# Performance work log

Measured on AMD Instinct MI355X. Metric: run time of the kernel, lower is better.

The kernel has to match this reference:

```python
import jax, jax.numpy as jnp
import numpy as np

TOP_K = 2

def setup_inputs() -> dict:
    key = jax.random.key(0)
    ks = jax.random.split(key, 8)
    B, T, C, E, I, S = 1, 2048, 2048, 8, 1408, 2816
    s = 0.02  # weight scale for numerical stability
    return {
        "x": jax.random.normal(ks[0], (B, T, C), jnp.float32),
        "gate_w": jax.random.normal(ks[1], (E, C), jnp.float32) * s,
        "w1": jax.random.normal(ks[2], (E, I, C), jnp.float32) * s,
        "w3": jax.random.normal(ks[3], (E, I, C), jnp.float32) * s,
        "w2": jax.random.normal(ks[4], (E, C, I), jnp.float32) * s,
        "sw1": jax.random.normal(ks[5], (S, C), jnp.float32) * s,
        "sw3": jax.random.normal(ks[6], (S, C), jnp.float32) * s,
        "sw2": jax.random.normal(ks[7], (C, S), jnp.float32) * s,
    }

def reference(x, gate_w, w1, w3, w2, sw1, sw3, sw2):
    B, T, C = x.shape
    E = gate_w.shape[0]
    xf = x.reshape(-1, C)                      # [N, C]
    N = xf.shape[0]
    # --- routing: top-k of raw logits, softmax over the k selected logits ---
    logits = xf @ gate_w.T                     # [N, E]
    pv, idx = jax.lax.top_k(logits, TOP_K)     # [N, K]
    pv = jax.nn.softmax(pv.astype(jnp.float32), axis=-1).astype(x.dtype)
    # token-expert combine weights (sum of probs per expert, scatter of top-k)
    tew = jnp.zeros((N, E), x.dtype).at[jnp.arange(N)[:, None], idx].add(pv)
    # --- experts (SwiGLU), computed densely over all experts and masked by tew ---
    h = jax.nn.silu(jnp.einsum('nc,eic->nei', xf, w1)) * jnp.einsum('nc,eic->nei', xf, w3)
    eo = jnp.einsum('nei,eci->nec', h, w2)     # [N, E, C]
    y = jnp.einsum('nec,ne->nc', eo, tew).reshape(B, T, C)
    # --- shared expert on the residual input ---
    sh = (jax.nn.silu(x @ sw1.T) * (x @ sw3.T)) @ sw2.T
    return y + sh
```

## Files before the change

### kernel.cpp

```cpp
#include <hip/hip_runtime.h>

#define DEVI __device__ __forceinline__

typedef __attribute__((ext_vector_type(4))) float f32x4;
typedef __attribute__((ext_vector_type(8))) short bf16x8;

static constexpr int NT = 2048;
static constexpr int CD = 2048;
static constexpr int NE = 8;
static constexpr int ID = 1408;
static constexpr int SD = 2816;
static constexpr int ROWS = 2 * NT;
static constexpr int ROWS_PAD = ROWS + 256;

DEVI unsigned short f2bf(float f) {
  unsigned u = __builtin_bit_cast(unsigned, f);
  u += 0x7fff + ((u >> 16) & 1);
  return (unsigned short)(u >> 16);
}
DEVI float bf2f(unsigned short s) { return __builtin_bit_cast(float, (unsigned)s << 16); }
DEVI float silu_f(float z) { return z / (1.f + __expf(-z)); }

DEVI void gll16(const void* g, void* l) {
  __builtin_amdgcn_global_load_lds((__attribute__((address_space(1))) void*)(void*)g,
                                   (__attribute__((address_space(3))) void*)l, 16, 0, 0);
}

DEVI void bar_sched() {
  __builtin_amdgcn_s_barrier();
  __builtin_amdgcn_sched_barrier(0);
}
DEVI void sched0() { __builtin_amdgcn_sched_barrier(0); }
DEVI void wait_vm8() { asm volatile("s_waitcnt vmcnt(8)" ::: "memory"); }
DEVI void wait_vm0() { asm volatile("s_waitcnt vmcnt(0)" ::: "memory"); }
DEVI void wait_lgk0() { asm volatile("s_waitcnt lgkmcnt(0)" ::: "memory"); }

DEVI int swz8(int bid, int nwg) {
  constexpr int CH = 8, G = 64;
  int nfull = nwg - (nwg % G);
  if (bid >= nfull) return bid;
  int c = bid / G, r = bid % G;
  return c * G + (r % 8) * CH + (r / 8);
}
DEVI int swz_chunk(int bid, int nwg) {
  constexpr int CH = 16, G = 8 * CH;
  int nfull = nwg - (nwg % G);
  if (bid >= nfull) return bid;
  int c = bid / G, r = bid % G;
  return c * G + (r % 8) * CH + (r / 8);
}

__global__ __launch_bounds__(256) void k_cvt(const float* __restrict__ s,
                                             unsigned short* __restrict__ d, int n8)
{
  int i = blockIdx.x * 256 + threadIdx.x;
  int stride = gridDim.x * 256;
  for (; i < n8; i += stride) {
    float4 a = ((const float4*)s)[2 * i];
    float4 b = ((const float4*)s)[2 * i + 1];
    ushort4 p0 = make_ushort4(f2bf(a.x), f2bf(a.y), f2bf(a.z), f2bf(a.w));
    ushort4 p1 = make_ushort4(f2bf(b.x), f2bf(b.y), f2bf(b.z), f2bf(b.w));
    ((ushort4*)d)[2 * i]     = p0;
    ((ushort4*)d)[2 * i + 1] = p1;
  }
}

__global__ __launch_bounds__(64) void k_router(const float* __restrict__ x,
    const float* __restrict__ gw, int* __restrict__ counts,
    int* __restrict__ eidx, int* __restrict__ posn, float* __restrict__ probs)
{
  const int n = blockIdx.x;
  const int lane = threadIdx.x;
  const float4* xr = (const float4*)(x + (size_t)n * CD);
  float acc[NE];
#pragma unroll
  for (int e = 0; e < NE; ++e) acc[e] = 0.f;
  for (int i = lane; i < CD / 4; i += 64) {
    float4 xv = xr[i];
#pragma unroll
    for (int e = 0; e < NE; ++e) {
      float4 gv = ((const float4*)(gw + (size_t)e * CD))[i];
      acc[e] += xv.x * gv.x + xv.y * gv.y + xv.z * gv.z + xv.w * gv.w;
    }
  }
#pragma unroll
  for (int e = 0; e < NE; ++e) {
    float v = acc[e];
#pragma unroll
    for (int off = 32; off > 0; off >>= 1) v += __shfl_down(v, off);
    acc[e] = v;
  }
  if (lane == 0) {
    int b0 = 0; float m0 = acc[0];
#pragma unroll
    for (int e = 1; e < NE; ++e) if (acc[e] > m0) { m0 = acc[e]; b0 = e; }
    int b1 = -1; float m1 = 0.f;
#pragma unroll
    for (int e = 0; e < NE; ++e) {
      if (e == b0) continue;
      if (b1 < 0 || acc[e] > m1) { m1 = acc[e]; b1 = e; }
    }
    float d = __expf(m1 - m0);
    float inv = 1.f / (1.f + d);
    eidx[2 * n] = b0; eidx[2 * n + 1] = b1;
    probs[2 * n] = inv; probs[2 * n + 1] = d * inv;
    posn[2 * n] = atomicAdd(&counts[b0], 1);
    posn[2 * n + 1] = atomicAdd(&counts[b1], 1);
  }
}

__global__ void k_scan(const int* __restrict__ counts, int* __restrict__ bases) {
  if (threadIdx.x == 0) {
    int s = 0;
    for (int e = 0; e < NE; ++e) { bases[e] = s; s += counts[e]; }
  }
}

__global__ __launch_bounds__(256) void k_build(const int* __restrict__ eidx,
    const int* __restrict__ posn, const int* __restrict__ bases,
    int* __restrict__ rows_of, int* __restrict__ row2tok)
{
  int n = blockIdx.x * 256 + threadIdx.x;
  if (n >= NT) return;
#pragma unroll
  for (int k = 0; k < 2; ++k) {
    int e = eidx[2 * n + k];
    int row = bases[e] + posn[2 * n + k];
    rows_of[2 * n + k] = row;
    row2tok[row] = n;
  }
}

__global__ __launch_bounds__(512, 2) void k_up(
    const unsigned short* __restrict__ xb,
    const unsigned short* __restrict__ w1b, const unsigned short* __restrict__ w3b,
    const unsigned short* __restrict__ sw1b, const unsigned short* __restrict__ sw3b,
    unsigned short* __restrict__ h, unsigned short* __restrict__ hs,
    const int* __restrict__ counts, const int* __restrict__ bases,
    const int* __restrict__ row2tok)
{
  extern __shared__ char sm[];
  constexpr int NSH = (NT / 256) * (SD / 128);
  constexpr int NWG = NSH + NE * (ID / 128) * (NT / 256);
  constexpr int NSTEP = CD / 64;

  int lin = swz8((int)blockIdx.x, NWG);
  int cls, mx, pn, e = 0;
  if (lin < NSH) { cls = 0; mx = lin % 8; pn = lin / 8; }
  else { cls = 1; int r = lin - NSH; mx = r % 8; r /= 8; pn = r % 11; e = r / 11; }

  int M = NT, baserow = 0;
  if (cls) { M = counts[e]; if (mx * 256 >= M) return; baserow = bases[e]; }
  const int m0 = mx * 256, n0 = pn * 128;

  const unsigned short* B1 = cls ? w1b + ((size_t)e * ID + n0) * CD : sw1b + (size_t)n0 * CD;
  const unsigned short* B3 = cls ? w3b + ((size_t)e * ID + n0) * CD : sw3b + (size_t)n0 * CD;

  const int tid = threadIdx.x, l = tid & 63, w = tid >> 6;
  const int wr = w >> 2, wn = w & 3;
  const int slot = ((tid & 7) ^ ((tid >> 3) & 7)) * 16;

  const char* aP[4];
#pragma unroll
  for (int t = 0; t < 4; ++t) {
    int r = t * 64 + (tid >> 3);
    const unsigned short* rb;
    if (cls) {
      int grow = m0 + r; int gr = grow < M ? grow : 0;
      rb = xb + (size_t)row2tok[baserow + gr] * CD;
    } else {
      rb = xb + (size_t)(m0 + r) * CD;
    }
    aP[t] = (const char*)rb + slot;
  }
  const char* bP1[2]; const char* bP3[2];
#pragma unroll
  for (int t = 0; t < 2; ++t) {
    int r = t * 64 + (tid >> 3);
    bP1[t] = (const char*)(B1 + (size_t)r * CD) + slot;
    bP3[t] = (const char*)(B3 + (size_t)r * CD) + slot;
  }

  f32x4 acc1[8][2], acc3[8][2];
#pragma unroll
  for (int m = 0; m < 8; ++m)
#pragma unroll
    for (int n = 0; n < 2; ++n) {
      acc1[m][n] = {0.f, 0.f, 0.f, 0.f};
      acc3[m][n] = {0.f, 0.f, 0.f, 0.f};
    }

  const int lrow = l & 15, lkg = l >> 4, l7 = l & 7;

  auto stage_first = [&](char* base, size_t kb) {
#pragma unroll
    for (int t = 0; t < 4; ++t) gll16(aP[t] + kb, base + t * 8192 + tid * 16);
  };
  auto stage_second = [&](char* base, size_t kb) {
    char* sB1 = base + 32768; char* sB3 = base + 49152;
#pragma unroll
    for (int t = 0; t < 2; ++t) {
      gll16(bP1[t] + kb, sB1 + t * 8192 + tid * 16);
      gll16(bP3[t] + kb, sB3 + t * 8192 + tid * 16);
    }
  };
  auto ldq = [&](bf16x8* fa, bf16x8* fb1, bf16x8* fb3, const char* cur, int mh, int kk) {
    const char* sA = cur; const char* sB1 = cur + 32768; const char* sB3 = cur + 49152;
    const int ao = ((kk * 4 + lkg) ^ l7) * 16;
#pragma unroll
    for (int m = 0; m < 4; ++m)
      fa[m] = *(const bf16x8*)(sA + (wr * 128 + mh * 64 + m * 16 + lrow) * 128 + ao);
#pragma unroll
    for (int n = 0; n < 2; ++n) {
      fb1[n] = *(const bf16x8*)(sB1 + (wn * 32 + n * 16 + lrow) * 128 + ao);
      fb3[n] = *(const bf16x8*)(sB3 + (wn * 32 + n * 16 + lrow) * 128 + ao);
    }
  };
  auto mmq = [&](const bf16x8* fa, const bf16x8* fb1, const bf16x8* fb3, int mh) {
    __builtin_amdgcn_s_setprio(1);
#pragma unroll
    for (int n = 0; n < 2; ++n)
#pragma unroll
      for (int m = 0; m < 4; ++m) {
        acc1[mh * 4 + m][n] = __builtin_amdgcn_mfma_f32_16x16x32_bf16(fa[m], fb1[n], acc1[mh * 4 + m][n], 0, 0, 0);
        acc3[mh * 4 + m][n] = __builtin_amdgcn_mfma_f32_16x16x32_bf16(fa[m], fb3[n], acc3[mh * 4 + m][n], 0, 0, 0);
      }
    __builtin_amdgcn_s_setprio(0);
  };

  stage_first(sm, 0);
  stage_second(sm, 0);
  wait_vm0(); bar_sched();

  bf16x8 Xa[4], Xb1[2], Xb3[2], Ya[4], Yb1[2], Yb3[2];

  for (int t = 0; t < NSTEP; ++t) {
    char* cur = sm + (size_t)(t & 1) * 65536;
    char* nxt = sm + (size_t)((t + 1) & 1) * 65536;
    size_t kb = (size_t)(t + 1) * 128;
    ldq(Xa, Xb1, Xb3, cur, 0, 0);
    sched0();
    if (t + 1 < NSTEP) stage_first(nxt, kb);
    ldq(Ya, Yb1, Yb3, cur, 1, 0);
    mmq(Xa, Xb1, Xb3, 0);
    sched0();
    if (t + 1 < NSTEP) stage_second(nxt, kb);
    ldq(Xa, Xb1, Xb3, cur, 0, 1);
    mmq(Ya, Yb1, Yb3, 1);
    sched0();
    ldq(Ya, Yb1, Yb3, cur, 1, 1);
    mmq(Xa, Xb1, Xb3, 0);
    sched0();
    mmq(Ya, Yb1, Yb3, 1);
    sched0();
    wait_vm0(); wait_lgk0();
    bar_sched();
  }

#pragma unroll
  for (int m = 0; m < 8; ++m) {
    int rb_ = m0 + wr * 128 + m * 16 + lkg * 4;
#pragma unroll
    for (int j = 0; j < 4; ++j) {
      int grow = rb_ + j;
      if (cls && grow >= M) continue;
#pragma unroll
      for (int n = 0; n < 2; ++n) {
        int gcol = n0 + wn * 32 + n * 16 + lrow;
        float hh = silu_f(acc1[m][n][j]) * acc3[m][n][j];
        if (cls) h[(size_t)(baserow + grow) * ID + gcol] = f2bf(hh);
        else     hs[(size_t)grow * SD + gcol] = f2bf(hh);
      }
    }
  }
}

struct GArgs {
  const unsigned short* A;
  const unsigned short* B1;
  void* Out;
  const int* counts; const int* bases;
  const int* rows_of; const float* probs; const unsigned short* eo;
};

template<int MODE>
__global__ __launch_bounds__(256) void k_gemm(GArgs a)
{
  constexpr int KD = (MODE == 1 ? ID : SD);
  constexpr int BN = 128;
  constexpr int NH = BN / 2;
  constexpr int NFT = NH / 16;
  constexpr int BT = 4;
  constexpr int NMB = NT / 128;
  constexpr int NPN = CD / 128;
  constexpr int NWG = NMB * NPN * ((MODE == 1) ? NE : 1);
  constexpr int NSTEP = KD / 64;

  __shared__ __align__(16) char smem[2][32768];

  int lin = swz_chunk((int)blockIdx.x, NWG);
  const int mx = lin % NMB; lin /= NMB;
  const int pn = lin % NPN;
  const int e  = lin / NPN;

  int M, baserow = 0;
  if constexpr (MODE == 1) {
    int ne = a.counts[e];
    if (mx * 128 >= ne) return;
    M = ne; baserow = a.bases[e];
  } else { M = NT; }
  const int m0 = mx * 128;
  const int n0 = pn * BN;

  const unsigned short* B1;
  if constexpr (MODE == 1) { B1 = a.B1 + ((size_t)e * CD + n0) * ID; }
  else                     { B1 = a.B1 + (size_t)n0 * SD; }

  const int tid = threadIdx.x, l = tid & 63, w = tid >> 6;
  const int wr = w >> 1, wc = w & 1;
  const int slot = ((l & 7) ^ ((l >> 3) & 7)) * 16;

  const char* aP[4];
#pragma unroll
  for (int t = 0; t < 4; ++t) {
    int r = w * 32 + t * 8 + (l >> 3);
    const unsigned short* rb;
    if constexpr (MODE == 1) {
      rb = a.A + (size_t)(baserow + m0 + r) * KD;
    } else {
      rb = a.A + (size_t)(m0 + r) * KD;
    }
    aP[t] = (const char*)rb + slot;
  }
  const char* bP1[BT];
#pragma unroll
  for (int t = 0; t < BT; ++t) {
    int r = w * (8 * BT) + t * 8 + (l >> 3);
    bP1[t] = (const char*)(B1 + (size_t)r * KD) + slot;
  }

  f32x4 acc1[4][NFT];
#pragma unroll
  for (int m = 0; m < 4; ++m)
#pragma unroll
    for (int n = 0; n < NFT; ++n) acc1[m][n] = {0.f, 0.f, 0.f, 0.f};

  const int lrow = l & 15, lkg = l >> 4, l7 = l & 7;
  const int ao0 = (lkg ^ l7) * 16;
  const int ao1 = ((4 + lkg) ^ l7) * 16;

  auto stageF = [&](char* base, size_t kb) {
    char* sA = base; char* sB1 = base + 16384;
#pragma unroll
    for (int t = 0; t < 4; ++t) gll16(aP[t] + kb, sA + (w * 4 + t) * 1024);
#pragma unroll
    for (int t = 0; t < BT; ++t) gll16(bP1[t] + kb, sB1 + (w * BT + t) * 1024);
  };
  auto computeF = [&](const char* base) {
    const char* sA = base; const char* sB1 = base + 16384;
#pragma unroll
    for (int kk = 0; kk < 2; ++kk) {
      const int ao = kk ? ao1 : ao0;
      bf16x8 af[4];
#pragma unroll
      for (int m = 0; m < 4; ++m)
        af[m] = *(const bf16x8*)(sA + (wr * 64 + m * 16 + lrow) * 128 + ao);
#pragma unroll
      for (int n = 0; n < NFT; ++n) {
        bf16x8 b1 = *(const bf16x8*)(sB1 + (wc * NH + n * 16 + lrow) * 128 + ao);
#pragma unroll
        for (int m = 0; m < 4; ++m)
          acc1[m][n] = __builtin_amdgcn_mfma_f32_16x16x32_bf16(af[m], b1, acc1[m][n], 0, 0, 0);
      }
    }
  };

  stageF(smem[0], 0);
  int t = 0;
  for (; t < NSTEP - 2; t += 2) {
    stageF(smem[1], (size_t)(t + 1) * 128);
    wait_vm8(); bar_sched();
    computeF(smem[0]);
    wait_lgk0(); bar_sched();
    stageF(smem[0], (size_t)(t + 2) * 128);
    wait_vm8(); bar_sched();
    computeF(smem[1]);
    wait_lgk0(); bar_sched();
  }
  stageF(smem[1], (size_t)(NSTEP - 1) * 128);
  wait_vm8(); bar_sched();
  computeF(smem[0]);
  wait_vm0(); bar_sched();
  computeF(smem[1]);

#pragma unroll
  for (int m = 0; m < 4; ++m) {
    int rbase = m0 + wr * 64 + m * 16 + lkg * 4;
#pragma unroll
    for (int j = 0; j < 4; ++j) {
      int grow = rbase + j;
      if constexpr (MODE == 1) { if (grow >= M) continue; }
      int r0 = 0, r1 = 0; float p0 = 0.f, p1 = 0.f;
      if constexpr (MODE == 3) {
        r0 = a.rows_of[2 * grow]; r1 = a.rows_of[2 * grow + 1];
        p0 = a.probs[2 * grow];   p1 = a.probs[2 * grow + 1];
      }
#pragma unroll
      for (int n = 0; n < NFT; ++n) {
        int gcol = n0 + wc * NH + n * 16 + lrow;
        float v1 = acc1[m][n][j];
        if constexpr (MODE == 1) {
          ((unsigned short*)a.Out)[(size_t)(baserow + grow) * CD + gcol] = f2bf(v1);
        } else {
          float vv = v1 + p0 * bf2f(a.eo[(size_t)r0 * CD + gcol]) + p1 * bf2f(a.eo[(size_t)r1 * CD + gcol]);
          ((float*)a.Out)[(size_t)grow * CD + gcol] = vv;
        }
      }
    }
  }
}

extern "C" void kernel_launch(void* const* d_in, const int* in_sizes, int n_in,
                              void* d_out, int out_size, void* d_ws, size_t ws_size,
                              hipStream_t stream)
{
  const float* x   = (const float*)d_in[0];
  const float* gw  = (const float*)d_in[1];
  const float* w1  = (const float*)d_in[2];
  const float* w3  = (const float*)d_in[3];
  const float* w2  = (const float*)d_in[4];
  const float* sw1 = (const float*)d_in[5];
  const float* sw3 = (const float*)d_in[6];
  const float* sw2 = (const float*)d_in[7];
  float* y = (float*)d_out;

  char* p = (char*)d_ws;
  auto alloc = [&](size_t b) { char* r = p; p += (b + 255) & ~(size_t)255; return r; };
  int*   counts  = (int*)alloc(NE * 4);
  int*   bases   = (int*)alloc(NE * 4);
  int*   eidx    = (int*)alloc((size_t)NT * 2 * 4);
  int*   posn    = (int*)alloc((size_t)NT * 2 * 4);
  float* probs   = (float*)alloc((size_t)NT * 2 * 4);
  int*   rows_of = (int*)alloc((size_t)NT * 2 * 4);
  int*   row2tok = (int*)alloc((size_t)ROWS * 4);
  unsigned short* xb   = (unsigned short*)alloc((size_t)NT * CD * 2);
  unsigned short* w1b  = (unsigned short*)alloc((size_t)NE * ID * CD * 2);
  unsigned short* w3b  = (unsigned short*)alloc((size_t)NE * ID * CD * 2);
  unsigned short* w2b  = (unsigned short*)alloc((size_t)NE * CD * ID * 2);
  unsigned short* sw1b = (unsigned short*)alloc((size_t)SD * CD * 2);
  unsigned short* sw3b = (unsigned short*)alloc((size_t)SD * CD * 2);
  unsigned short* sw2b = (unsigned short*)alloc((size_t)CD * SD * 2);
  unsigned short* h    = (unsigned short*)alloc((size_t)ROWS_PAD * ID * 2);
  unsigned short* eo   = (unsigned short*)alloc((size_t)ROWS_PAD * CD * 2);
  unsigned short* hs   = (unsigned short*)alloc((size_t)NT * SD * 2);

  hipFuncSetAttribute((const void*)k_up, hipFuncAttributeMaxDynamicSharedMemorySize, 131072);

  hipMemsetAsync(counts, 0, NE * 4, stream);

  auto cvt = [&](const float* s, unsigned short* d, size_t n) {
    int n8 = (int)(n / 8);
    int grid = (n8 + 255) / 256; if (grid > 2048) grid = 2048;
    k_cvt<<<grid, 256, 0, stream>>>(s, d, n8);
  };
  cvt(x,   xb,   (size_t)NT * CD);
  cvt(w1,  w1b,  (size_t)NE * ID * CD);
  cvt(w3,  w3b,  (size_t)NE * ID * CD);
  cvt(w2,  w2b,  (size_t)NE * CD * ID);
  cvt(sw1, sw1b, (size_t)SD * CD);
  cvt(sw3, sw3b, (size_t)SD * CD);
  cvt(sw2, sw2b, (size_t)CD * SD);

  k_router<<<NT, 64, 0, stream>>>(x, gw, counts, eidx, posn, probs);
  k_scan<<<1, 64, 0, stream>>>(counts, bases);
  k_build<<<NT / 256, 256, 0, stream>>>(eidx, posn, bases, rows_of, row2tok);

  {
    constexpr int NWG = (NT / 256) * (SD / 128) + NE * (ID / 128) * (NT / 256);
    k_up<<<NWG, 512, 131072, stream>>>(xb, w1b, w3b, sw1b, sw3b, h, hs,
                                       counts, bases, row2tok);
  }
  {
    GArgs g{}; g.A = h; g.B1 = w2b; g.Out = eo;
    g.counts = counts; g.bases = bases;
    k_gemm<1><<<(NT / 128) * (CD / 128) * NE, 256, 0, stream>>>(g);
  }
  {
    GArgs g{}; g.A = hs; g.B1 = sw2b; g.Out = y;
    g.rows_of = rows_of; g.probs = probs; g.eo = eo;
    k_gemm<3><<<(NT / 128) * (CD / 128), 256, 0, stream>>>(g);
  }
}
```

Baseline: 411.4 us.

## Merge weight conversions into one launch and reshape up-projection warp tiling and prefetch

The seven fp32-to-bf16 conversion launches become one grid-stride kernel that finds each element's segment from a prefix table, which removes launch gaps and tail effects. In the fused up-projection kernel, the 8 waves move from a 2x4 to a 4x2 layout, so each wave now owns a 64x64 tile and A/B fragments are reused more evenly. The K-loop prefetch is also restructured: A tiles are staged two steps ahead with a partial vmcnt wait, and B tiles one step ahead. The cost is extra barriers per step, more live registers, and some risk that the wait counts do not match the loads actually in flight.

```diff
diff --git a/kernel.cpp b/kernel.cpp
--- a/kernel.cpp
+++ b/kernel.cpp
@@ -32,6 +32,7 @@
 }
 DEVI void sched0() { __builtin_amdgcn_sched_barrier(0); }
 DEVI void wait_vm8() { asm volatile("s_waitcnt vmcnt(8)" ::: "memory"); }
+DEVI void wait_vm4() { asm volatile("s_waitcnt vmcnt(4)" ::: "memory"); }
 DEVI void wait_vm0() { asm volatile("s_waitcnt vmcnt(0)" ::: "memory"); }
 DEVI void wait_lgk0() { asm volatile("s_waitcnt lgkmcnt(0)" ::: "memory"); }
 
@@ -50,18 +51,26 @@
   return c * G + (r % 8) * CH + (r / 8);
 }
 
-__global__ __launch_bounds__(256) void k_cvt(const float* __restrict__ s,
-                                             unsigned short* __restrict__ d, int n8)
+struct Cvt7 {
+  const float* s[7];
+  unsigned short* d[7];
+  long long beg[8];
+};
+__global__ __launch_bounds__(256) void k_cvt7(Cvt7 c)
 {
-  int i = blockIdx.x * 256 + threadIdx.x;
-  int stride = gridDim.x * 256;
-  for (; i < n8; i += stride) {
-    float4 a = ((const float4*)s)[2 * i];
-    float4 b = ((const float4*)s)[2 * i + 1];
+  const long long total = c.beg[7];
+  const long long stride = (long long)gridDim.x * 256;
+  for (long long i = (long long)blockIdx.x * 256 + threadIdx.x; i < total; i += stride) {
+    int sg = 0;
+#pragma unroll
+    for (int k = 1; k < 7; ++k) if (i >= c.beg[k]) sg = k;
+    long long j = i - c.beg[sg];
+    float4 a = ((const float4*)c.s[sg])[2 * j];
+    float4 b = ((const float4*)c.s[sg])[2 * j + 1];
     ushort4 p0 = make_ushort4(f2bf(a.x), f2bf(a.y), f2bf(a.z), f2bf(a.w));
     ushort4 p1 = make_ushort4(f2bf(b.x), f2bf(b.y), f2bf(b.z), f2bf(b.w));
-    ((ushort4*)d)[2 * i]     = p0;
-    ((ushort4*)d)[2 * i + 1] = p1;
+    ((ushort4*)c.d[sg])[2 * j]     = p0;
+    ((ushort4*)c.d[sg])[2 * j + 1] = p1;
   }
 }
 
@@ -157,7 +166,7 @@
   const unsigned short* B3 = cls ? w3b + ((size_t)e * ID + n0) * CD : sw3b + (size_t)n0 * CD;
 
   const int tid = threadIdx.x, l = tid & 63, w = tid >> 6;
-  const int wr = w >> 2, wn = w & 3;
+  const int wr = w >> 1, wn = w & 1;
   const int slot = ((tid & 7) ^ ((tid >> 3) & 7)) * 16;
 
   const char* aP[4];
@@ -181,22 +190,22 @@
     bP3[t] = (const char*)(B3 + (size_t)r * CD) + slot;
   }
 
-  f32x4 acc1[8][2], acc3[8][2];
-#pragma unroll
-  for (int m = 0; m < 8; ++m)
-#pragma unroll
-    for (int n = 0; n < 2; ++n) {
+  f32x4 acc1[4][4], acc3[4][4];
+#pragma unroll
+  for (int m = 0; m < 4; ++m)
+#pragma unroll
+    for (int n = 0; n < 4; ++n) {
       acc1[m][n] = {0.f, 0.f, 0.f, 0.f};
       acc3[m][n] = {0.f, 0.f, 0.f, 0.f};
     }
 
   const int lrow = l & 15, lkg = l >> 4, l7 = l & 7;
 
-  auto stage_first = [&](char* base, size_t kb) {
+  auto stageA = [&](char* base, size_t kb) {
 #pragma unroll
     for (int t = 0; t < 4; ++t) gll16(aP[t] + kb, base + t * 8192 + tid * 16);
   };
-  auto stage_second = [&](char* base, size_t kb) {
+  auto stageB = [&](char* base, size_t kb) {
     char* sB1 = base + 32768; char* sB3 = base + 49152;
 #pragma unroll
     for (int t = 0; t < 2; ++t) {
@@ -204,69 +213,72 @@
       gll16(bP3[t] + kb, sB3 + t * 8192 + tid * 16);
     }
   };
-  auto ldq = [&](bf16x8* fa, bf16x8* fb1, bf16x8* fb3, const char* cur, int mh, int kk) {
-    const char* sA = cur; const char* sB1 = cur + 32768; const char* sB3 = cur + 49152;
+  auto ldA = [&](bf16x8* fa, const char* cur, int kk) {
     const int ao = ((kk * 4 + lkg) ^ l7) * 16;
 #pragma unroll
     for (int m = 0; m < 4; ++m)
-      fa[m] = *(const bf16x8*)(sA + (wr * 128 + mh * 64 + m * 16 + lrow) * 128 + ao);
-#pragma unroll
-    for (int n = 0; n < 2; ++n) {
-      fb1[n] = *(const bf16x8*)(sB1 + (wn * 32 + n * 16 + lrow) * 128 + ao);
-      fb3[n] = *(const bf16x8*)(sB3 + (wn * 32 + n * 16 + lrow) * 128 + ao);
-    }
-  };
-  auto mmq = [&](const bf16x8* fa, const bf16x8* fb1, const bf16x8* fb3, int mh) {
+      fa[m] = *(const bf16x8*)(cur + (wr * 64 + m * 16 + lrow) * 128 + ao);
+  };
+  auto ldB = [&](bf16x8* fb1, bf16x8* fb3, const char* cur, int kk) {
+    const char* sB1 = cur + 32768; const char* sB3 = cur + 49152;
+    const int ao = ((kk * 4 + lkg) ^ l7) * 16;
+#pragma unroll
+    for (int n = 0; n < 4; ++n) {
+      fb1[n] = *(const bf16x8*)(sB1 + (wn * 64 + n * 16 + lrow) * 128 + ao);
+      fb3[n] = *(const bf16x8*)(sB3 + (wn * 64 + n * 16 + lrow) * 128 + ao);
+    }
+  };
+  auto mmq = [&](const bf16x8* fa, const bf16x8* fb1, const bf16x8* fb3) {
     __builtin_amdgcn_s_setprio(1);
 #pragma unroll
-    for (int n = 0; n < 2; ++n)
+    for (int n = 0; n < 4; ++n)
 #pragma unroll
       for (int m = 0; m < 4; ++m) {
-        acc1[mh * 4 + m][n] = __builtin_amdgcn_mfma_f32_16x16x32_bf16(fa[m], fb1[n], acc1[mh * 4 + m][n], 0, 0, 0);
-        acc3[mh * 4 + m][n] = __builtin_amdgcn_mfma_f32_16x16x32_bf16(fa[m], fb3[n], acc3[mh * 4 + m][n], 0, 0, 0);
+        acc1[m][n] = __builtin_amdgcn_mfma_f32_16x16x32_bf16(fa[m], fb1[n], acc1[m][n], 0, 0, 0);
+        acc3[m][n] = __builtin_amdgcn_mfma_f32_16x16x32_bf16(fa[m], fb3[n], acc3[m][n], 0, 0, 0);
       }
     __builtin_amdgcn_s_setprio(0);
   };
 
-  stage_first(sm, 0);
-  stage_second(sm, 0);
-  wait_vm0(); bar_sched();
-
-  bf16x8 Xa[4], Xb1[2], Xb3[2], Ya[4], Yb1[2], Yb3[2];
+  stageA(sm, 0); stageB(sm, 0);
+  stageA(sm + 65536, 128);
+  wait_vm4(); bar_sched();
 
   for (int t = 0; t < NSTEP; ++t) {
-    char* cur = sm + (size_t)(t & 1) * 65536;
+    const char* cur = sm + (size_t)(t & 1) * 65536;
     char* nxt = sm + (size_t)((t + 1) & 1) * 65536;
-    size_t kb = (size_t)(t + 1) * 128;
-    ldq(Xa, Xb1, Xb3, cur, 0, 0);
+    const bool pf  = (t + 1 < NSTEP);
+    const bool pf2 = (t + 2 < NSTEP);
+    bf16x8 Fa0[4], Fa1[4], Fb1[4], Fb3[4];
+    ldA(Fa0, cur, 0);
+    ldA(Fa1, cur, 1);
+    if (pf) stageB(nxt, (size_t)(t + 1) * 128);
     sched0();
-    if (t + 1 < NSTEP) stage_first(nxt, kb);
-    ldq(Ya, Yb1, Yb3, cur, 1, 0);
-    mmq(Xa, Xb1, Xb3, 0);
+    ldB(Fb1, Fb3, cur, 0);
+    mmq(Fa0, Fb1, Fb3);
     sched0();
-    if (t + 1 < NSTEP) stage_second(nxt, kb);
-    ldq(Xa, Xb1, Xb3, cur, 0, 1);
-    mmq(Ya, Yb1, Yb3, 1);
+    ldB(Fb1, Fb3, cur, 1);
+    mmq(Fa1, Fb1, Fb3);
     sched0();
-    ldq(Ya, Yb1, Yb3, cur, 1, 1);
-    mmq(Xa, Xb1, Xb3, 0);
-    sched0();
-    mmq(Ya, Yb1, Yb3, 1);
-    sched0();
-    wait_vm0(); wait_lgk0();
-    bar_sched();
-  }
-
-#pragma unroll
-  for (int m = 0; m < 8; ++m) {
-    int rb_ = m0 + wr * 128 + m * 16 + lkg * 4;
+    if (pf) {
+      wait_lgk0();
+      bar_sched();
+      if (pf2) stageA((char*)cur, (size_t)(t + 2) * 128);
+      if (pf2) wait_vm4(); else wait_vm0();
+      bar_sched();
+    }
+  }
+
+#pragma unroll
+  for (int m = 0; m < 4; ++m) {
+    int rb_ = m0 + wr * 64 + m * 16 + lkg * 4;
 #pragma unroll
     for (int j = 0; j < 4; ++j) {
       int grow = rb_ + j;
       if (cls && grow >= M) continue;
 #pragma unroll
-      for (int n = 0; n < 2; ++n) {
-        int gcol = n0 + wn * 32 + n * 16 + lrow;
+      for (int n = 0; n < 4; ++n) {
+        int gcol = n0 + wn * 64 + n * 16 + lrow;
         float hh = silu_f(acc1[m][n][j]) * acc3[m][n][j];
         if (cls) h[(size_t)(baserow + grow) * ID + gcol] = f2bf(hh);
         else     hs[(size_t)grow * SD + gcol] = f2bf(hh);
@@ -458,18 +470,20 @@
 
   hipMemsetAsync(counts, 0, NE * 4, stream);
 
-  auto cvt = [&](const float* s, unsigned short* d, size_t n) {
-    int n8 = (int)(n / 8);
-    int grid = (n8 + 255) / 256; if (grid > 2048) grid = 2048;
-    k_cvt<<<grid, 256, 0, stream>>>(s, d, n8);
-  };
-  cvt(x,   xb,   (size_t)NT * CD);
-  cvt(w1,  w1b,  (size_t)NE * ID * CD);
-  cvt(w3,  w3b,  (size_t)NE * ID * CD);
-  cvt(w2,  w2b,  (size_t)NE * CD * ID);
-  cvt(sw1, sw1b, (size_t)SD * CD);
-  cvt(sw3, sw3b, (size_t)SD * CD);
-  cvt(sw2, sw2b, (size_t)CD * SD);
+  {
+    Cvt7 c{};
+    const float* ss[7] = {x, w1, w3, w2, sw1, sw3, sw2};
+    unsigned short* dd[7] = {xb, w1b, w3b, w2b, sw1b, sw3b, sw2b};
+    size_t nn[7] = {(size_t)NT * CD, (size_t)NE * ID * CD, (size_t)NE * ID * CD,
+                    (size_t)NE * CD * ID, (size_t)SD * CD, (size_t)SD * CD,
+                    (size_t)CD * SD};
+    long long acc = 0;
+    for (int k = 0; k < 7; ++k) {
+      c.s[k] = ss[k]; c.d[k] = dd[k]; c.beg[k] = acc; acc += (long long)(nn[k] / 8);
+    }
+    c.beg[7] = acc;
+    k_cvt7<<<2048, 256, 0, stream>>>(c);
+  }
 
   k_router<<<NT, 64, 0, stream>>>(x, gw, counts, eidx, posn, probs);
   k_scan<<<1, 64, 0, stream>>>(counts, bases);
```

Measured after the change: 418.7 us. No clear change (+1.8%).
